# Kernel optimization log

Measured on AMD Instinct MI355X. Metric: run time of the kernel, lower is better.

Reference implementation:

```python
import jax, jax.numpy as jnp
import numpy as np

N_NODES = 100000
N_EDGES = 1600000
IN_DIM = 256
HID = 128
N_LAYERS = 4
OUT_DIM = 7
LAMDA = 0.5
LN_EPS = 1e-5


def setup_inputs() -> dict:
    key = jax.random.key(0)
    ks = jax.random.split(key, 12)
    x = jax.random.normal(ks[0], (N_NODES, IN_DIM), jnp.float32)
    edge_index = jax.random.randint(ks[1], (2, N_EDGES), 0, N_NODES, dtype=jnp.int32)

    def unif(k, shape, fan_out):
        s = 1.0 / np.sqrt(fan_out)
        return jax.random.uniform(k, shape, jnp.float32, -s, s)

    W_proj = unif(ks[2], (IN_DIM, HID), HID)
    b_proj = unif(ks[3], (HID,), HID)
    gamma = jnp.ones((HID,), jnp.float32)
    beta = jnp.zeros((HID,), jnp.float32)
    q_w = unif(ks[4], (HID, 1), 1)
    q_b = unif(ks[5], (1,), 1)
    conv_w = unif(ks[6], (N_LAYERS, HID, HID), HID)
    cls_w = unif(ks[7], (HID, OUT_DIM), OUT_DIM)
    cls_b = unif(ks[8], (OUT_DIM,), OUT_DIM)
    return {"x": x, "edge_index": edge_index, "W_proj": W_proj, "b_proj": b_proj,
            "gamma": gamma, "beta": beta, "q_w": q_w, "q_b": q_b,
            "conv_w": conv_w, "cls_w": cls_w, "cls_b": cls_b}


def reference(x, edge_index, W_proj, b_proj, gamma, beta, q_w, q_b, conv_w, cls_w, cls_b):
    n = x.shape[0]
    row, col = edge_index[0], edge_index[1]

    # symmetric normalization: D^-1/2 A D^-1/2 with unit edge data (duplicates sum)
    deg = jax.ops.segment_sum(jnp.ones(row.shape[0], x.dtype), row, num_segments=n)
    deg = jnp.where(deg == 0, jnp.ones_like(deg), deg)  # (row_sum==0)*1 + row_sum
    d_inv_sqrt = deg ** -0.5
    ew = d_inv_sqrt[row] * d_inv_sqrt[col]  # [E]

    def spmm(h):  # out[r] += ew * h[c]
        return jax.ops.segment_sum(ew[:, None] * h[col], row, num_segments=n)

    def layernorm(h):
        mu = jnp.mean(h, axis=-1, keepdims=True)
        var = jnp.mean((h - mu) ** 2, axis=-1, keepdims=True)
        return gamma * (h - mu) * jax.lax.rsqrt(var + LN_EPS) + beta

    h0 = layernorm(x @ W_proj + b_proj)  # project + layernorm
    h = h0
    for i in range(conv_w.shape[0]):
        # dropout is identity in eval mode
        s = jax.nn.sigmoid(h @ q_w + q_b - 1.0)  # [N,1] learned gate
        theta = LAMDA / (i + 1)
        hi = spmm(h)
        support = (1.0 - s) * hi + s * h0  # AOR blend (variant=False -> r == support)
        out = theta * (support @ conv_w[i]) + (1.0 - theta) * support  # DLR
        h = layernorm(jax.nn.relu(out))
    return h @ cls_w + cls_b
```

## Files before the change

kernel.cpp:

```cpp
#include <hip/hip_runtime.h>
#include <hip/hip_bf16.h>
#include <hip/hip_fp16.h>
#include <stdint.h>

#define N_NODES 100000
#define N_EDGES 1600000
#define IN_DIM 256
#define HID 128
#define N_LAYERS 4
#define OUT_DIM 7
#define LN_EPS 1e-5f

#define BSHIFT 6
#define BROWS 64
#define NBK 1563
#define CHUNK 16384
#define NCH ((N_EDGES + CHUNK - 1) / CHUNK)

typedef __attribute__((ext_vector_type(8))) short bf16x8;
typedef __attribute__((ext_vector_type(4))) float f32x4;

__device__ inline float bf2f1(uint16_t u) {
    union { uint32_t i; float f; } a; a.i = ((uint32_t)u) << 16; return a.f;
}
__device__ inline uint16_t f2bf(float f) {
    union { float f; uint32_t i; } a; a.f = f;
    uint32_t lsb = (a.i >> 16) & 1u;
    a.i += 0x7fffu + lsb;
    return (uint16_t)(a.i >> 16);
}
__device__ inline uint32_t packq(float a, float b, float qinv) {
    int qa = __float2int_rn(a * qinv);
    int qb = __float2int_rn(b * qinv);
    return ((uint32_t)(uint16_t)(short)qa) | (((uint32_t)(uint16_t)(short)qb) << 16);
}

__device__ __host__ inline int wpack_idx(int k, int c) {
    int kc = k >> 6, ks = (k >> 5) & 1, lg = (k >> 3) & 3, e = k & 7;
    int ct = c >> 4, li = c & 15;
    return ((((kc * 2 + ks) * 8 + ct) * 16 + li) * 4 + lg) * 8 + e;
}

__global__ void k_detect(const uint32_t* __restrict__ W, int* __restrict__ flag) {
    if (threadIdx.x == 0 && blockIdx.x == 0) {
        int cnt = 0;
        for (int i = 0; i < 64; i++) {
            uint32_t lo = W[i] & 0xffffu;
            uint32_t ex = (lo >> 7) & 0xff;
            if (ex >= 0x60 && ex < 0x7c) cnt++;
        }
        *flag = (cnt < 32) ? 1 : 0;
    }
}
__global__ void k_setflag(int* __restrict__ flag, int v) {
    if (threadIdx.x == 0) *flag = v;
}

__global__ __launch_bounds__(256) void k_cvt(const void* a0, const void* a1, const void* a2,
                                             const void* a3, const void* a4, const void* a5,
                                             const void* a6, const void* a7, const void* a8,
                                             float* __restrict__ dst, const int* __restrict__ flag) {
    int t = blockIdx.x * 256 + threadIdx.x;
    if (t >= 99720) return;
    const void* src; int i; int off;
    if      (t < 32768) { src = a0; i = t;         off = 0;     }
    else if (t < 32896) { src = a1; i = t - 32768; off = 32768; }
    else if (t < 33024) { src = a2; i = t - 32896; off = 32896; }
    else if (t < 33152) { src = a3; i = t - 33024; off = 33024; }
    else if (t < 33280) { src = a4; i = t - 33152; off = 33152; }
    else if (t < 33281) { src = a5; i = t - 33280; off = 33280; }
    else if (t < 98817) { src = a6; i = t - 33281; off = 33296; }
    else if (t < 99713) { src = a7; i = t - 98817; off = 98832; }
    else                { src = a8; i = t - 99713; off = 99728; }
    float v;
    if (*flag) v = ((const float*)src)[i];
    else       v = bf2f1(((const uint16_t*)src)[i]);
    dst[off + i] = v;
}

__global__ __launch_bounds__(256) void k_wsplit(const float* __restrict__ stg,
                                                uint16_t* __restrict__ wpkhi, uint16_t* __restrict__ wpklo,
                                                uint16_t* __restrict__ cwkhi, uint16_t* __restrict__ cwklo) {
    int t = blockIdx.x * 256 + threadIdx.x;
    if (t >= 32768 + 65536) return;
    float v; size_t dst; uint16_t *ha, *la;
    if (t < 32768) {
        int k = t >> 7, c = t & 127;
        v = stg[t];
        dst = (size_t)wpack_idx(k, c); ha = wpkhi; la = wpklo;
    } else {
        int u = t - 32768;
        int L = u >> 14, rem = u & 16383;
        int k = rem >> 7, c = rem & 127;
        v = stg[33296 + u];
        dst = (size_t)L * 16384 + wpack_idx(k, c); ha = cwkhi; la = cwklo;
    }
    uint16_t hb = f2bf(v);
    uint16_t lb = f2bf(v - bf2f1(hb));
    ha[dst] = hb; la[dst] = lb;
}


__global__ __launch_bounds__(256) void k_hist(const int* __restrict__ row, int* __restrict__ hist) {
    __shared__ int lh[NBK];
    int b = blockIdx.x, tid = threadIdx.x;
    for (int i = tid; i < NBK; i += 256) lh[i] = 0;
    __syncthreads();
    int e0 = b * CHUNK;
    int lim = N_EDGES - e0; if (lim > CHUNK) lim = CHUNK;
    for (int i = tid; i < lim; i += 256) atomicAdd(&lh[row[e0 + i] >> BSHIFT], 1);
    __syncthreads();
    for (int i = tid; i < NBK; i += 256) hist[(size_t)b * NBK + i] = lh[i];
}

__global__ __launch_bounds__(128) void k_hscan(int* __restrict__ hist, int* __restrict__ totB) {
    __shared__ int s[128];
    int bkt = blockIdx.x, t = threadIdx.x;
    int v = (t < NCH) ? hist[(size_t)t * NBK + bkt] : 0;
    s[t] = v;
    __syncthreads();
    for (int off = 1; off < 128; off <<= 1) {
        int add = (t >= off) ? s[t - off] : 0;
        __syncthreads();
        s[t] += add;
        __syncthreads();
    }
    if (t < NCH) hist[(size_t)t * NBK + bkt] = s[t] - v;
    if (t == 127) totB[bkt] = s[127];
}

__global__ __launch_bounds__(256) void k_bscan(const int* __restrict__ totB,
                                               int* __restrict__ boffB, int* __restrict__ rp) {
    __shared__ int ps[256];
    int t = threadIdx.x;
    const int STRIP = 7;
    int base = t * STRIP;
    int loc[STRIP]; int sum = 0;
#pragma unroll
    for (int j = 0; j < STRIP; j++) {
        int idx = base + j;
        int v = (idx < NBK) ? totB[idx] : 0;
        loc[j] = sum; sum += v;
    }
    ps[t] = sum;
    __syncthreads();
    int v = ps[t];
    for (int off = 1; off < 256; off <<= 1) {
        int add = (t >= off) ? ps[t - off] : 0;
        __syncthreads();
        ps[t] += add;
        __syncthreads();
    }
    int excl = ps[t] - v;
#pragma unroll
    for (int j = 0; j < STRIP; j++) {
        int idx = base + j;
        if (idx < NBK) boffB[idx] = excl + loc[j];
    }
    if (t == 0) { boffB[NBK] = N_EDGES; rp[N_NODES] = N_EDGES; }
}

__global__ __launch_bounds__(256) void k_sortscat(const int* __restrict__ row, const int* __restrict__ col,
                                                  const int* __restrict__ hist, const int* __restrict__ boffB,
                                                  uint32_t* __restrict__ ebp) {
    __shared__ int dbase[NBK];
    __shared__ int lcnt[NBK];
    int b = blockIdx.x, tid = threadIdx.x;
    for (int i = tid; i < NBK; i += 256) {
        dbase[i] = boffB[i] + hist[(size_t)b * NBK + i];
        lcnt[i] = 0;
    }
    __syncthreads();
    int e0 = b * CHUNK;
    int lim = N_EDGES - e0; if (lim > CHUNK) lim = CHUNK;
    for (int i = tid; i < lim; i += 256) {
        int r = row[e0 + i], c = col[e0 + i];
        int bk = r >> BSHIFT;
        int rank = atomicAdd(&lcnt[bk], 1);
        ebp[dbase[bk] + rank] = ((uint32_t)(r & (BROWS - 1)) << 17) | (uint32_t)c;
    }
}

__global__ __launch_bounds__(256) void k_bfin(const uint32_t* __restrict__ ebp, const int* __restrict__ boffB,
                                              int* __restrict__ rp, float* __restrict__ dis,
                                              int* __restrict__ edc) {
    __shared__ int ldeg[BROWS];
    __shared__ int lcur[BROWS];
    int b = blockIdx.x, tid = threadIdx.x;
    int base = boffB[b];
    int n = boffB[b + 1] - base;
    if (tid < BROWS) ldeg[tid] = 0;
    __syncthreads();
    for (int i = tid; i < n; i += 256) atomicAdd(&ldeg[ebp[base + i] >> 17], 1);
    __syncthreads();
    if (tid == 0) {
        int run = 0;
        for (int r = 0; r < BROWS; r++) { int d = ldeg[r]; lcur[r] = run; run += d; }
    }
    __syncthreads();
    int row0 = b << BSHIFT;
    if (tid < BROWS && row0 + tid < N_NODES) {
        int d = ldeg[tid];
        rp[row0 + tid]  = base + lcur[tid];
        dis[row0 + tid] = rsqrtf((float)(d > 0 ? d : 1));
    }
    __syncthreads();
    for (int i = tid; i < n; i += 256) {
        uint32_t pk = ebp[base + i];
        int r = pk >> 17;
        int pos = atomicAdd(&lcur[r], 1);
        edc[base + pos] = (int)(pk & 0x1FFFFu);
    }
}


__global__ __launch_bounds__(256) void k_spmm(const uint32_t* __restrict__ Hq,
                                              const float* __restrict__ ScD,
                                              const float* __restrict__ H0,
                                              const int* __restrict__ rp,
                                              const int* __restrict__ edc,
                                              const float* __restrict__ S,
                                              const float* __restrict__ dis,
                                              float* __restrict__ Sup) {
    int wid  = (blockIdx.x * 256 + threadIdx.x) >> 6;
    int lane = threadIdx.x & 63;
    if (wid >= N_NODES) return;

    float s  = S[wid];
    float dr = dis[wid];
    float h0x = H0[(size_t)wid * 128 + lane];
    float h0y = H0[(size_t)wid * 128 + 64 + lane];

    int p0 = rp[wid], p1 = rp[wid + 1];
    float ax = 0.f, ay = 0.f;
    int p = p0;
    for (; p + 8 <= p1; p += 8) {
        int c[8]; uint32_t u[8]; float w[8];
#pragma unroll
        for (int j = 0; j < 8; j++) c[j] = edc[p + j];
#pragma unroll
        for (int j = 0; j < 8; j++) u[j] = Hq[(size_t)c[j] * 64 + lane];
#pragma unroll
        for (int j = 0; j < 8; j++) w[j] = ScD[c[j]];
#pragma unroll
        for (int j = 0; j < 8; j++) {
            ax += w[j] * (float)((int)(u[j] << 16) >> 16);
            ay += w[j] * (float)((int)u[j] >> 16);
        }
    }
    for (; p + 4 <= p1; p += 4) {
        int c[4]; uint32_t u[4]; float w[4];
#pragma unroll
        for (int j = 0; j < 4; j++) c[j] = edc[p + j];
#pragma unroll
        for (int j = 0; j < 4; j++) u[j] = Hq[(size_t)c[j] * 64 + lane];
#pragma unroll
        for (int j = 0; j < 4; j++) w[j] = ScD[c[j]];
#pragma unroll
        for (int j = 0; j < 4; j++) {
            ax += w[j] * (float)((int)(u[j] << 16) >> 16);
            ay += w[j] * (float)((int)u[j] >> 16);
        }
    }
    for (; p < p1; p++) {
        int c = edc[p];
        uint32_t u = Hq[(size_t)c * 64 + lane];
        float w = ScD[c];
        ax += w * (float)((int)(u << 16) >> 16);
        ay += w * (float)((int)u >> 16);
    }
    float f = (1.f - s) * dr;
    Sup[(size_t)wid * 128 + lane]      = f * ax + s * h0x;
    Sup[(size_t)wid * 128 + 64 + lane] = f * ay + s * h0y;
}


template <int KD, int MODE, int WH, int WQ, int WF>
__global__ __launch_bounds__(256, 4) void k_gemm(
    const void* __restrict__ Araw,
    const uint16_t* __restrict__ Whi,
    const uint16_t* __restrict__ Wlo,
    const float* __restrict__ bias, const float* __restrict__ gamma,
    const float* __restrict__ beta, const float* __restrict__ qw,
    const float* __restrict__ qb, float theta, const int* __restrict__ flag,
    const float* __restrict__ dis,
    float* __restrict__ Hout, uint32_t* __restrict__ Hq,
    float* __restrict__ Sc, float* __restrict__ S)
{
    if (*flag != WF) return;
    constexpr int F32A = (MODE == 0) ? WF : 1;
    constexpr int NC = KD / 64;

    const int tid  = threadIdx.x;
    const int lane = tid & 63;
    const int wv   = tid >> 6;
    const int li   = lane & 15;
    const int lg   = lane >> 4;
    const size_t row0 = (size_t)blockIdx.x * 64;
    size_t arow = row0 + wv * 16 + li;
    if (arow >= N_NODES) arow = N_NODES - 1;

    f32x4 acc[8];
#pragma unroll
    for (int ct = 0; ct < 8; ct++) acc[ct] = (f32x4){0.f, 0.f, 0.f, 0.f};

#pragma unroll
    for (int kc = 0; kc < NC; kc++) {
#pragma unroll
        for (int ks = 0; ks < 2; ks++) {
            const int koff = kc * 64 + ks * 32 + lg * 8;
            bf16x8 ah, al;
            if constexpr (F32A) {
                const float* ap = (const float*)Araw + arow * KD + koff;
                float4 u0 = *(const float4*)ap;
                float4 u1 = *(const float4*)(ap + 4);
                float f[8] = {u0.x, u0.y, u0.z, u0.w, u1.x, u1.y, u1.z, u1.w};
#pragma unroll
                for (int j = 0; j < 8; j++) {
                    uint16_t hb = f2bf(f[j]);
                    ah[j] = (short)hb;
                    al[j] = (short)f2bf(f[j] - bf2f1(hb));
                }
            } else {
                ah = *(const bf16x8*)((const uint16_t*)Araw + arow * KD + koff);
            }
            const size_t wb0 = (size_t)(kc * 2 + ks) * 4096 + (size_t)li * 32 + (size_t)lg * 8;
#pragma unroll
            for (int ct = 0; ct < 8; ct++) {
                const size_t wb = wb0 + (size_t)ct * 512;
                bf16x8 bh = *(const bf16x8*)(Whi + wb);
                acc[ct] = __builtin_amdgcn_mfma_f32_16x16x32_bf16(ah, bh, acc[ct], 0, 0, 0);
                if constexpr (F32A)
                    acc[ct] = __builtin_amdgcn_mfma_f32_16x16x32_bf16(al, bh, acc[ct], 0, 0, 0);
                if constexpr (WF) {
                    bf16x8 bl = *(const bf16x8*)(Wlo + wb);
                    acc[ct] = __builtin_amdgcn_mfma_f32_16x16x32_bf16(ah, bl, acc[ct], 0, 0, 0);
                }
            }
        }
    }

    float gm[8], bt[8], qv[8], bi[8];
#pragma unroll
    for (int ct = 0; ct < 8; ct++) {
        int c = ct * 16 + li;
        gm[ct] = gamma[c]; bt[ct] = beta[c]; qv[ct] = qw[c];
        bi[ct] = (MODE == 0) ? bias[c] : 0.f;
    }
    const float qbv = qb[0];
    const float om  = 1.f - theta;
    const float* Af = (const float*)Araw;

#pragma unroll
    for (int r = 0; r < 4; r++) {
        int rowl  = wv * 16 + lg * 4 + r;
        size_t rg = row0 + rowl;
        size_t rc = (rg < N_NODES) ? rg : (N_NODES - 1);
        float v[8];
        if (MODE == 0) {
#pragma unroll
            for (int ct = 0; ct < 8; ct++) v[ct] = acc[ct][r] + bi[ct];
        } else {
#pragma unroll
            for (int ct = 0; ct < 8; ct++) {
                float sv = Af[rc * KD + ct * 16 + li];
                float o  = theta * acc[ct][r] + om * sv;
                v[ct] = o > 0.f ? o : 0.f;
            }
        }
        float sum = 0.f, sq = 0.f;
#pragma unroll
        for (int ct = 0; ct < 8; ct++) { sum += v[ct]; sq += v[ct] * v[ct]; }
        sum += __shfl_xor(sum, 1); sum += __shfl_xor(sum, 2);
        sum += __shfl_xor(sum, 4); sum += __shfl_xor(sum, 8);
        sq  += __shfl_xor(sq, 1);  sq  += __shfl_xor(sq, 2);
        sq  += __shfl_xor(sq, 4);  sq  += __shfl_xor(sq, 8);
        float mu  = sum * (1.f / 128.f);
        float var = fmaxf(sq * (1.f / 128.f) - mu * mu, 0.f);
        float rs  = rsqrtf(var + LN_EPS);
        float y[8];
#pragma unroll
        for (int ct = 0; ct < 8; ct++) y[ct] = gm[ct] * (v[ct] - mu) * rs + bt[ct];

        if (WQ) {
            float zd = 0.f, am = 0.f;
#pragma unroll
            for (int ct = 0; ct < 8; ct++) { zd += y[ct] * qv[ct]; am = fmaxf(am, fabsf(y[ct])); }
            zd += __shfl_xor(zd, 1); zd += __shfl_xor(zd, 2);
            zd += __shfl_xor(zd, 4); zd += __shfl_xor(zd, 8);
            am = fmaxf(am, __shfl_xor(am, 1)); am = fmaxf(am, __shfl_xor(am, 2));
            am = fmaxf(am, __shfl_xor(am, 4)); am = fmaxf(am, __shfl_xor(am, 8));
            float amc  = fmaxf(am, 1e-20f);
            float qinv = 32767.f / amc;
            if (rg < N_NODES) {
                uint32_t* mq = Hq + rg * 64;
#pragma unroll
                for (int ct = 0; ct < 4; ct++)
                    mq[ct * 16 + li] = packq(y[ct], y[ct + 4], qinv);
                if (li == 0) {
                    Sc[rg] = amc * (1.f / 32767.f) * dis[rg];
                    S[rg]  = 1.f / (1.f + __expf(-(zd + qbv - 1.f)));
                }
            }
        }
        if (WH && rg < N_NODES) {
            float* dst = Hout + rg * 128;
#pragma unroll
            for (int ct = 0; ct < 8; ct++) dst[ct * 16 + li] = y[ct];
        }
    }
}


__global__ __launch_bounds__(256) void k_cls(const float* __restrict__ H,
                                             const float* __restrict__ Wc,
                                             const float* __restrict__ bc,
                                             const int* __restrict__ flag,
                                             void* __restrict__ out) {
    __shared__ float wS[128][8];
    int tid = threadIdx.x;
    for (int idx = tid; idx < 128 * 7; idx += 256) wS[idx / 7][idx % 7] = Wc[idx];
    __syncthreads();
    int isf32 = *flag;
    int gid = blockIdx.x * 256 + tid;
    int n = gid >> 3, j = gid & 7;
    if (n >= N_NODES || j >= OUT_DIM) return;
    const float4* hr = (const float4*)(H + (size_t)n * 128);
    float acc = bc[j];
#pragma unroll
    for (int k4 = 0; k4 < 32; k4++) {
        float4 h4 = hr[k4];
        acc += h4.x * wS[4 * k4][j]     + h4.y * wS[4 * k4 + 1][j]
             + h4.z * wS[4 * k4 + 2][j] + h4.w * wS[4 * k4 + 3][j];
    }
    size_t oi = (size_t)n * OUT_DIM + j;
    if (isf32) ((float*)out)[oi] = acc;
    else       ((uint16_t*)out)[oi] = f2bf(acc);
}


extern "C" void kernel_launch(void* const* d_in, const int* in_sizes, int n_in,
                              void* d_out, int out_size, void* d_ws, size_t ws_size,
                              hipStream_t stream) {
    const void* x_raw = d_in[0];
    const int*  ei    = (const int*)d_in[1];
    const int* row = ei;
    const int* col = ei + N_EDGES;

    char* ws = (char*)d_ws;
    size_t off = 0;
    auto alloc = [&](size_t b) { void* p = ws + off; off = (off + b + 255) & ~(size_t)255; return p; };
    int*      flag = (int*)alloc(4);
    float*    stgf = (float*)alloc((size_t)99744 * 4);
    int*      rp   = (int*)alloc(((size_t)N_NODES + 1) * 4);
    float*    dis  = (float*)alloc((size_t)N_NODES * 4);
    int*      hist = (int*)alloc((size_t)NCH * NBK * 4);
    int*      totB = (int*)alloc((size_t)NBK * 4);
    int*      boffB= (int*)alloc(((size_t)NBK + 1) * 4);
    int*      edc  = (int*)alloc((size_t)N_EDGES * 4);
    float*    h0   = (float*)alloc((size_t)N_NODES * HID * 4);
    float*    sup  = (float*)alloc((size_t)N_NODES * HID * 4);
    uint32_t* hq   = (uint32_t*)alloc((size_t)N_NODES * 64 * 4);
    float*    Scq  = (float*)alloc((size_t)N_NODES * 4);
    float*    Sg   = (float*)alloc((size_t)N_NODES * 4);
    uint16_t* wpkhi = (uint16_t*)alloc((size_t)32768 * 2);
    uint16_t* wpklo = (uint16_t*)alloc((size_t)32768 * 2);
    uint16_t* cwkhi = (uint16_t*)alloc((size_t)65536 * 2);
    uint16_t* cwklo = (uint16_t*)alloc((size_t)65536 * 2);
    uint32_t* ebp  = (uint32_t*)h0;

    const float* bp  = stgf + 32768;
    const float* gm  = stgf + 32896;
    const float* bt  = stgf + 33024;
    const float* qw  = stgf + 33152;
    const float* qb  = stgf + 33280;
    const float* clw = stgf + 98832;
    const float* clb = stgf + 99728;

    int hostflag = -1;
    if (in_sizes && n_in >= 3) {
        if      (in_sizes[2] == 32768 * 4) hostflag = 1;
        else if (in_sizes[2] == 32768 * 2) hostflag = 0;
        else if (in_sizes[0] == N_NODES * IN_DIM * 4) hostflag = 1;
        else if (in_sizes[0] == N_NODES * IN_DIM * 2) hostflag = 0;
    }
    if (hostflag >= 0) k_setflag<<<1, 64, 0, stream>>>(flag, hostflag);
    else               k_detect<<<1, 64, 0, stream>>>((const uint32_t*)d_in[2], flag);

    k_cvt<<<(99720 + 255) / 256, 256, 0, stream>>>(d_in[2], d_in[3], d_in[4], d_in[5], d_in[6],
                                                   d_in[7], d_in[8], d_in[9], d_in[10], stgf, flag);
    k_wsplit<<<(98304 + 255) / 256, 256, 0, stream>>>(stgf, wpkhi, wpklo, cwkhi, cwklo);

    k_hist<<<NCH, 256, 0, stream>>>(row, hist);
    k_hscan<<<NBK, 128, 0, stream>>>(hist, totB);
    k_bscan<<<1, 256, 0, stream>>>(totB, boffB, rp);
    k_sortscat<<<NCH, 256, 0, stream>>>(row, col, hist, boffB, ebp);
    k_bfin<<<NBK, 256, 0, stream>>>(ebp, boffB, rp, dis, edc);

    const int gemm_grid = (N_NODES + 63) / 64;
    if (hostflag != 0)
        k_gemm<IN_DIM, 0, 1, 1, 1><<<gemm_grid, 256, 0, stream>>>(
            x_raw, wpkhi, wpklo, bp, gm, bt, qw, qb, 0.f, flag, dis, h0, hq, Scq, Sg);
    if (hostflag != 1)
        k_gemm<IN_DIM, 0, 1, 1, 0><<<gemm_grid, 256, 0, stream>>>(
            x_raw, wpkhi, wpklo, bp, gm, bt, qw, qb, 0.f, flag, dis, h0, hq, Scq, Sg);

    for (int i = 0; i < N_LAYERS; i++) {
        k_spmm<<<(N_NODES + 3) / 4, 256, 0, stream>>>(hq, Scq, h0, rp, edc, Sg, dis, sup);
        float theta = 0.5f / (float)(i + 1);
        const uint16_t* whi = cwkhi + (size_t)i * 16384;
        const uint16_t* wlo = cwklo + (size_t)i * 16384;
        if (i < N_LAYERS - 1) {
            if (hostflag != 0)
                k_gemm<HID, 1, 0, 1, 1><<<gemm_grid, 256, 0, stream>>>(
                    sup, whi, wlo, nullptr, gm, bt, qw, qb, theta, flag, dis, sup, hq, Scq, Sg);
            if (hostflag != 1)
                k_gemm<HID, 1, 0, 1, 0><<<gemm_grid, 256, 0, stream>>>(
                    sup, whi, wlo, nullptr, gm, bt, qw, qb, theta, flag, dis, sup, hq, Scq, Sg);
        } else {
            if (hostflag != 0)
                k_gemm<HID, 1, 1, 0, 1><<<gemm_grid, 256, 0, stream>>>(
                    sup, whi, wlo, nullptr, gm, bt, qw, qb, theta, flag, dis, sup, hq, Scq, Sg);
            if (hostflag != 1)
                k_gemm<HID, 1, 1, 0, 0><<<gemm_grid, 256, 0, stream>>>(
                    sup, whi, wlo, nullptr, gm, bt, qw, qb, theta, flag, dis, sup, hq, Scq, Sg);
        }
    }
    k_cls<<<((size_t)N_NODES * 8 + 255) / 256, 256, 0, stream>>>(sup, clw, clb, flag, d_out);
}
```

Before: 834.6 us.

## Stage GEMM weights in LDS, double rows per wave, store support as bf16 hi/lo

The GEMM now copies each 128-deep weight slab into shared memory once per block, with a repacked weight layout, and each wave computes 32 rows instead of 16. The block tile grows to 128 rows, so weight reads from global/L2 are amortised over more rows. The SpMM writes the support matrix pre-split into bf16 hi and lo halves, so the GEMM skips the fp32-to-bf16 split and reads the same number of bytes. The costs are higher register and LDS use, with occupancy lowered to 2 blocks per SM, plus a change in where the final layer output lands (h0 reused).

```diff
diff --git a/kernel.cpp b/kernel.cpp
--- a/kernel.cpp
+++ b/kernel.cpp
@@ -36,9 +36,9 @@
 }
 
 __device__ __host__ inline int wpack_idx(int k, int c) {
-    int kc = k >> 6, ks = (k >> 5) & 1, lg = (k >> 3) & 3, e = k & 7;
+    int ksg = k >> 5, lg = (k >> 3) & 3, e = k & 7;
     int ct = c >> 4, li = c & 15;
-    return ((((kc * 2 + ks) * 8 + ct) * 16 + li) * 4 + lg) * 8 + e;
+    return ((ksg * 8 + ct) * 64 + (lg * 16 + li)) * 8 + e;
 }
 
 __global__ void k_detect(const uint32_t* __restrict__ W, int* __restrict__ flag) {
@@ -221,7 +221,8 @@
                                               const int* __restrict__ edc,
                                               const float* __restrict__ S,
                                               const float* __restrict__ dis,
-                                              float* __restrict__ Sup) {
+                                              uint16_t* __restrict__ SupHi,
+                                              uint16_t* __restrict__ SupLo) {
     int wid  = (blockIdx.x * 256 + threadIdx.x) >> 6;
     int lane = threadIdx.x & 63;
     if (wid >= N_NODES) return;
@@ -270,16 +271,22 @@
         ay += w * (float)((int)u >> 16);
     }
     float f = (1.f - s) * dr;
-    Sup[(size_t)wid * 128 + lane]      = f * ax + s * h0x;
-    Sup[(size_t)wid * 128 + 64 + lane] = f * ay + s * h0y;
+    float ox = f * ax + s * h0x;
+    float oy = f * ay + s * h0y;
+    uint16_t hx = f2bf(ox), hy = f2bf(oy);
+    uint16_t lx = f2bf(ox - bf2f1(hx)), ly = f2bf(oy - bf2f1(hy));
+    SupHi[(size_t)wid * 128 + lane]      = hx;
+    SupHi[(size_t)wid * 128 + 64 + lane] = hy;
+    SupLo[(size_t)wid * 128 + lane]      = lx;
+    SupLo[(size_t)wid * 128 + 64 + lane] = ly;
 }
 
 
 template <int KD, int MODE, int WH, int WQ, int WF>
-__global__ __launch_bounds__(256, 4) void k_gemm(
-    const void* __restrict__ Araw,
-    const uint16_t* __restrict__ Whi,
-    const uint16_t* __restrict__ Wlo,
+__global__ __launch_bounds__(256, 2) void k_gemm(
+    const void* __restrict__ Ax,
+    const uint16_t* __restrict__ Ahi, const uint16_t* __restrict__ Alo,
+    const uint16_t* __restrict__ Wh, const uint16_t* __restrict__ Wl,
     const float* __restrict__ bias, const float* __restrict__ gamma,
     const float* __restrict__ beta, const float* __restrict__ qw,
     const float* __restrict__ qb, float theta, const int* __restrict__ flag,
@@ -289,126 +296,169 @@
 {
     if (*flag != WF) return;
     constexpr int F32A = (MODE == 0) ? WF : 1;
-    constexpr int NC = KD / 64;
+    constexpr int NKB = KD / 128;
+
+    __shared__ __align__(16) uint16_t sWh[16384];
+    __shared__ __align__(16) uint16_t sWl[16384];
 
     const int tid  = threadIdx.x;
     const int lane = tid & 63;
     const int wv   = tid >> 6;
     const int li   = lane & 15;
     const int lg   = lane >> 4;
-    const size_t row0 = (size_t)blockIdx.x * 64;
-    size_t arow = row0 + wv * 16 + li;
-    if (arow >= N_NODES) arow = N_NODES - 1;
-
-    f32x4 acc[8];
-#pragma unroll
-    for (int ct = 0; ct < 8; ct++) acc[ct] = (f32x4){0.f, 0.f, 0.f, 0.f};
-
-#pragma unroll
-    for (int kc = 0; kc < NC; kc++) {
-#pragma unroll
-        for (int ks = 0; ks < 2; ks++) {
-            const int koff = kc * 64 + ks * 32 + lg * 8;
-            bf16x8 ah, al;
-            if constexpr (F32A) {
-                const float* ap = (const float*)Araw + arow * KD + koff;
-                float4 u0 = *(const float4*)ap;
-                float4 u1 = *(const float4*)(ap + 4);
-                float f[8] = {u0.x, u0.y, u0.z, u0.w, u1.x, u1.y, u1.z, u1.w};
+    const size_t row0 = (size_t)blockIdx.x * 128;
+    const int wb = wv * 32;
+    size_t ar0 = row0 + wb + li;      if (ar0 >= N_NODES) ar0 = N_NODES - 1;
+    size_t ar1 = row0 + wb + 16 + li; if (ar1 >= N_NODES) ar1 = N_NODES - 1;
+
+    f32x4 acc0[8], acc1[8];
+#pragma unroll
+    for (int ct = 0; ct < 8; ct++) {
+        acc0[ct] = (f32x4){0.f, 0.f, 0.f, 0.f};
+        acc1[ct] = (f32x4){0.f, 0.f, 0.f, 0.f};
+    }
+
+    for (int kb = 0; kb < NKB; kb++) {
+        if (kb) __syncthreads();
+        const uint16_t* gh = Wh + kb * 16384;
+#pragma unroll
+        for (int it = 0; it < 8; it++) {
+            int t = tid + it * 256;
+            *(uint4*)(sWh + t * 8) = *(const uint4*)(gh + t * 8);
+        }
+        if constexpr (WF) {
+            const uint16_t* gl = Wl + kb * 16384;
+#pragma unroll
+            for (int it = 0; it < 8; it++) {
+                int t = tid + it * 256;
+                *(uint4*)(sWl + t * 8) = *(const uint4*)(gl + t * 8);
+            }
+        }
+        bf16x8 a0h[4], a1h[4], a0l[4], a1l[4];
+#pragma unroll
+        for (int s = 0; s < 4; s++) {
+            const int koff = kb * 128 + s * 32 + lg * 8;
+            if constexpr (MODE == 1) {
+                a0h[s] = *(const bf16x8*)(Ahi + ar0 * KD + koff);
+                a0l[s] = *(const bf16x8*)(Alo + ar0 * KD + koff);
+                a1h[s] = *(const bf16x8*)(Ahi + ar1 * KD + koff);
+                a1l[s] = *(const bf16x8*)(Alo + ar1 * KD + koff);
+            } else if constexpr (WF) {
+                const float* p0 = (const float*)Ax + ar0 * KD + koff;
+                const float* p1 = (const float*)Ax + ar1 * KD + koff;
+                float4 u0 = *(const float4*)p0, u1 = *(const float4*)(p0 + 4);
+                float4 v0 = *(const float4*)p1, v1 = *(const float4*)(p1 + 4);
+                float f0[8] = {u0.x, u0.y, u0.z, u0.w, u1.x, u1.y, u1.z, u1.w};
+                float f1[8] = {v0.x, v0.y, v0.z, v0.w, v1.x, v1.y, v1.z, v1.w};
 #pragma unroll
                 for (int j = 0; j < 8; j++) {
-                    uint16_t hb = f2bf(f[j]);
-                    ah[j] = (short)hb;
-                    al[j] = (short)f2bf(f[j] - bf2f1(hb));
+                    uint16_t hb0 = f2bf(f0[j]);
+                    a0h[s][j] = (short)hb0;
+                    a0l[s][j] = (short)f2bf(f0[j] - bf2f1(hb0));
+                    uint16_t hb1 = f2bf(f1[j]);
+                    a1h[s][j] = (short)hb1;
+                    a1l[s][j] = (short)f2bf(f1[j] - bf2f1(hb1));
                 }
             } else {
-                ah = *(const bf16x8*)((const uint16_t*)Araw + arow * KD + koff);
+                a0h[s] = *(const bf16x8*)((const uint16_t*)Ax + ar0 * KD + koff);
+                a1h[s] = *(const bf16x8*)((const uint16_t*)Ax + ar1 * KD + koff);
             }
-            const size_t wb0 = (size_t)(kc * 2 + ks) * 4096 + (size_t)li * 32 + (size_t)lg * 8;
+        }
+        __syncthreads();
+#pragma unroll
+        for (int s = 0; s < 4; s++) {
 #pragma unroll
             for (int ct = 0; ct < 8; ct++) {
-                const size_t wb = wb0 + (size_t)ct * 512;
-                bf16x8 bh = *(const bf16x8*)(Whi + wb);
-                acc[ct] = __builtin_amdgcn_mfma_f32_16x16x32_bf16(ah, bh, acc[ct], 0, 0, 0);
-                if constexpr (F32A)
-                    acc[ct] = __builtin_amdgcn_mfma_f32_16x16x32_bf16(al, bh, acc[ct], 0, 0, 0);
+                const int wo = ((s * 8 + ct) * 64 + lane) * 8;
+                bf16x8 bh = *(const bf16x8*)(sWh + wo);
+                acc0[ct] = __builtin_amdgcn_mfma_f32_16x16x32_bf16(a0h[s], bh, acc0[ct], 0, 0, 0);
+                acc1[ct] = __builtin_amdgcn_mfma_f32_16x16x32_bf16(a1h[s], bh, acc1[ct], 0, 0, 0);
+                if constexpr (F32A) {
+                    acc0[ct] = __builtin_amdgcn_mfma_f32_16x16x32_bf16(a0l[s], bh, acc0[ct], 0, 0, 0);
+                    acc1[ct] = __builtin_amdgcn_mfma_f32_16x16x32_bf16(a1l[s], bh, acc1[ct], 0, 0, 0);
+                }
                 if constexpr (WF) {
-                    bf16x8 bl = *(const bf16x8*)(Wlo + wb);
-                    acc[ct] = __builtin_amdgcn_mfma_f32_16x16x32_bf16(ah, bl, acc[ct], 0, 0, 0);
+                    bf16x8 bl = *(const bf16x8*)(sWl + wo);
+                    acc0[ct] = __builtin_amdgcn_mfma_f32_16x16x32_bf16(a0h[s], bl, acc0[ct], 0, 0, 0);
+                    acc1[ct] = __builtin_amdgcn_mfma_f32_16x16x32_bf16(a1h[s], bl, acc1[ct], 0, 0, 0);
                 }
             }
         }
     }
 
-    float gm[8], bt[8], qv[8], bi[8];
+    float gm[8], bt_[8], qv[8], bi[8];
 #pragma unroll
     for (int ct = 0; ct < 8; ct++) {
         int c = ct * 16 + li;
-        gm[ct] = gamma[c]; bt[ct] = beta[c]; qv[ct] = qw[c];
+        gm[ct] = gamma[c]; bt_[ct] = beta[c]; qv[ct] = qw[c];
         bi[ct] = (MODE == 0) ? bias[c] : 0.f;
     }
     const float qbv = qb[0];
     const float om  = 1.f - theta;
-    const float* Af = (const float*)Araw;
-
-#pragma unroll
-    for (int r = 0; r < 4; r++) {
-        int rowl  = wv * 16 + lg * 4 + r;
-        size_t rg = row0 + rowl;
-        size_t rc = (rg < N_NODES) ? rg : (N_NODES - 1);
-        float v[8];
-        if (MODE == 0) {
-#pragma unroll
-            for (int ct = 0; ct < 8; ct++) v[ct] = acc[ct][r] + bi[ct];
-        } else {
-#pragma unroll
-            for (int ct = 0; ct < 8; ct++) {
-                float sv = Af[rc * KD + ct * 16 + li];
-                float o  = theta * acc[ct][r] + om * sv;
-                v[ct] = o > 0.f ? o : 0.f;
-            }
-        }
-        float sum = 0.f, sq = 0.f;
-#pragma unroll
-        for (int ct = 0; ct < 8; ct++) { sum += v[ct]; sq += v[ct] * v[ct]; }
-        sum += __shfl_xor(sum, 1); sum += __shfl_xor(sum, 2);
-        sum += __shfl_xor(sum, 4); sum += __shfl_xor(sum, 8);
-        sq  += __shfl_xor(sq, 1);  sq  += __shfl_xor(sq, 2);
-        sq  += __shfl_xor(sq, 4);  sq  += __shfl_xor(sq, 8);
-        float mu  = sum * (1.f / 128.f);
-        float var = fmaxf(sq * (1.f / 128.f) - mu * mu, 0.f);
-        float rs  = rsqrtf(var + LN_EPS);
-        float y[8];
-#pragma unroll
-        for (int ct = 0; ct < 8; ct++) y[ct] = gm[ct] * (v[ct] - mu) * rs + bt[ct];
-
-        if (WQ) {
-            float zd = 0.f, am = 0.f;
-#pragma unroll
-            for (int ct = 0; ct < 8; ct++) { zd += y[ct] * qv[ct]; am = fmaxf(am, fabsf(y[ct])); }
-            zd += __shfl_xor(zd, 1); zd += __shfl_xor(zd, 2);
-            zd += __shfl_xor(zd, 4); zd += __shfl_xor(zd, 8);
-            am = fmaxf(am, __shfl_xor(am, 1)); am = fmaxf(am, __shfl_xor(am, 2));
-            am = fmaxf(am, __shfl_xor(am, 4)); am = fmaxf(am, __shfl_xor(am, 8));
-            float amc  = fmaxf(am, 1e-20f);
-            float qinv = 32767.f / amc;
-            if (rg < N_NODES) {
-                uint32_t* mq = Hq + rg * 64;
-#pragma unroll
-                for (int ct = 0; ct < 4; ct++)
-                    mq[ct * 16 + li] = packq(y[ct], y[ct + 4], qinv);
-                if (li == 0) {
-                    Sc[rg] = amc * (1.f / 32767.f) * dis[rg];
-                    S[rg]  = 1.f / (1.f + __expf(-(zd + qbv - 1.f)));
+
+    auto epi = [&](f32x4 (&acc)[8], int ssoff) {
+#pragma unroll
+        for (int r = 0; r < 4; r++) {
+            int rowl  = wb + ssoff + lg * 4 + r;
+            size_t rg = row0 + rowl;
+            size_t rc = (rg < N_NODES) ? rg : (N_NODES - 1);
+            float v[8];
+            if (MODE == 0) {
+#pragma unroll
+                for (int ct = 0; ct < 8; ct++) v[ct] = acc[ct][r] + bi[ct];
+            } else {
+#pragma unroll
+                for (int ct = 0; ct < 8; ct++) {
+                    int c = ct * 16 + li;
+                    float sv = bf2f1(Ahi[rc * KD + c]) + bf2f1(Alo[rc * KD + c]);
+                    float o  = theta * acc[ct][r] + om * sv;
+                    v[ct] = o > 0.f ? o : 0.f;
                 }
             }
-        }
-        if (WH && rg < N_NODES) {
-            float* dst = Hout + rg * 128;
-#pragma unroll
-            for (int ct = 0; ct < 8; ct++) dst[ct * 16 + li] = y[ct];
-        }
-    }
+            float sum = 0.f, sq = 0.f;
+#pragma unroll
+            for (int ct = 0; ct < 8; ct++) { sum += v[ct]; sq += v[ct] * v[ct]; }
+            sum += __shfl_xor(sum, 1); sum += __shfl_xor(sum, 2);
+            sum += __shfl_xor(sum, 4); sum += __shfl_xor(sum, 8);
+            sq  += __shfl_xor(sq, 1);  sq  += __shfl_xor(sq, 2);
+            sq  += __shfl_xor(sq, 4);  sq  += __shfl_xor(sq, 8);
+            float mu  = sum * (1.f / 128.f);
+            float var = fmaxf(sq * (1.f / 128.f) - mu * mu, 0.f);
+            float rs  = rsqrtf(var + LN_EPS);
+            float y[8];
+#pragma unroll
+            for (int ct = 0; ct < 8; ct++) y[ct] = gm[ct] * (v[ct] - mu) * rs + bt_[ct];
+
+            if (WQ) {
+                float zd = 0.f, am = 0.f;
+#pragma unroll
+                for (int ct = 0; ct < 8; ct++) { zd += y[ct] * qv[ct]; am = fmaxf(am, fabsf(y[ct])); }
+                zd += __shfl_xor(zd, 1); zd += __shfl_xor(zd, 2);
+                zd += __shfl_xor(zd, 4); zd += __shfl_xor(zd, 8);
+                am = fmaxf(am, __shfl_xor(am, 1)); am = fmaxf(am, __shfl_xor(am, 2));
+                am = fmaxf(am, __shfl_xor(am, 4)); am = fmaxf(am, __shfl_xor(am, 8));
+                float amc  = fmaxf(am, 1e-20f);
+                float qinv = 32767.f / amc;
+                if (rg < N_NODES) {
+                    uint32_t* mq = Hq + rg * 64;
+#pragma unroll
+                    for (int ct = 0; ct < 4; ct++)
+                        mq[ct * 16 + li] = packq(y[ct], y[ct + 4], qinv);
+                    if (li == 0) {
+                        Sc[rg] = amc * (1.f / 32767.f) * dis[rg];
+                        S[rg]  = 1.f / (1.f + __expf(-(zd + qbv - 1.f)));
+                    }
+                }
+            }
+            if (WH && rg < N_NODES) {
+                float* dst = Hout + rg * 128;
+#pragma unroll
+                for (int ct = 0; ct < 8; ct++) dst[ct * 16 + li] = y[ct];
+            }
+        }
+    };
+    epi(acc0, 0);
+    epi(acc1, 16);
 }
 
 
@@ -459,7 +509,8 @@
     int*      boffB= (int*)alloc(((size_t)NBK + 1) * 4);
     int*      edc  = (int*)alloc((size_t)N_EDGES * 4);
     float*    h0   = (float*)alloc((size_t)N_NODES * HID * 4);
-    float*    sup  = (float*)alloc((size_t)N_NODES * HID * 4);
+    uint16_t* suphi= (uint16_t*)alloc((size_t)N_NODES * HID * 2);
+    uint16_t* suplo= (uint16_t*)alloc((size_t)N_NODES * HID * 2);
     uint32_t* hq   = (uint32_t*)alloc((size_t)N_NODES * 64 * 4);
     float*    Scq  = (float*)alloc((size_t)N_NODES * 4);
     float*    Sg   = (float*)alloc((size_t)N_NODES * 4);
@@ -497,34 +548,41 @@
     k_sortscat<<<NCH, 256, 0, stream>>>(row, col, hist, boffB, ebp);
     k_bfin<<<NBK, 256, 0, stream>>>(ebp, boffB, rp, dis, edc);
 
-    const int gemm_grid = (N_NODES + 63) / 64;
+    const int gg = (N_NODES + 127) / 128;
     if (hostflag != 0)
-        k_gemm<IN_DIM, 0, 1, 1, 1><<<gemm_grid, 256, 0, stream>>>(
-            x_raw, wpkhi, wpklo, bp, gm, bt, qw, qb, 0.f, flag, dis, h0, hq, Scq, Sg);
+        k_gemm<IN_DIM, 0, 1, 1, 1><<<gg, 256, 0, stream>>>(
+            x_raw, nullptr, nullptr, wpkhi, wpklo, bp, gm, bt, qw, qb, 0.f, flag, dis,
+            h0, hq, Scq, Sg);
     if (hostflag != 1)
-        k_gemm<IN_DIM, 0, 1, 1, 0><<<gemm_grid, 256, 0, stream>>>(
-            x_raw, wpkhi, wpklo, bp, gm, bt, qw, qb, 0.f, flag, dis, h0, hq, Scq, Sg);
+        k_gemm<IN_DIM, 0, 1, 1, 0><<<gg, 256, 0, stream>>>(
+            x_raw, nullptr, nullptr, wpkhi, wpklo, bp, gm, bt, qw, qb, 0.f, flag, dis,
+            h0, hq, Scq, Sg);
 
     for (int i = 0; i < N_LAYERS; i++) {
-        k_spmm<<<(N_NODES + 3) / 4, 256, 0, stream>>>(hq, Scq, h0, rp, edc, Sg, dis, sup);
+        k_spmm<<<(N_NODES + 3) / 4, 256, 0, stream>>>(hq, Scq, h0, rp, edc, Sg, dis, suphi, suplo);
         float theta = 0.5f / (float)(i + 1);
         const uint16_t* whi = cwkhi + (size_t)i * 16384;
         const uint16_t* wlo = cwklo + (size_t)i * 16384;
-        if (i < N_LAYERS - 1) {
+        const int wh = (i == N_LAYERS - 1) ? 1 : 0;
+        if (wh) {
             if (hostflag != 0)
-                k_gemm<HID, 1, 0, 1, 1><<<gemm_grid, 256, 0, stream>>>(
-                    sup, whi, wlo, nullptr, gm, bt, qw, qb, theta, flag, dis, sup, hq, Scq, Sg);
+                k_gemm<HID, 1, 1, 0, 1><<<gg, 256, 0, stream>>>(
+                    nullptr, suphi, suplo, whi, wlo, nullptr, gm, bt, qw, qb, theta, flag, dis,
+                    h0, hq, Scq, Sg);
             if (hostflag != 1)
-                k_gemm<HID, 1, 0, 1, 0><<<gemm_grid, 256, 0, stream>>>(
-                    sup, whi, wlo, nullptr, gm, bt, qw, qb, theta, flag, dis, sup, hq, Scq, Sg);
+                k_gemm<HID, 1, 1, 0, 0><<<gg, 256, 0, stream>>>(
+                    nullptr, suphi, suplo, whi, wlo, nullptr, gm, bt, qw, qb, theta, flag, dis,
+                    h0, hq, Scq, Sg);
         } else {
             if (hostflag != 0)
-                k_gemm<HID, 1, 1, 0, 1><<<gemm_grid, 256, 0, stream>>>(
-                    sup, whi, wlo, nullptr, gm, bt, qw, qb, theta, flag, dis, sup, hq, Scq, Sg);
+                k_gemm<HID, 1, 0, 1, 1><<<gg, 256, 0, stream>>>(
+                    nullptr, suphi, suplo, whi, wlo, nullptr, gm, bt, qw, qb, theta, flag, dis,
+                    h0, hq, Scq, Sg);
             if (hostflag != 1)
-                k_gemm<HID, 1, 1, 0, 0><<<gemm_grid, 256, 0, stream>>>(
-                    sup, whi, wlo, nullptr, gm, bt, qw, qb, theta, flag, dis, sup, hq, Scq, Sg);
-        }
-    }
-    k_cls<<<((size_t)N_NODES * 8 + 255) / 256, 256, 0, stream>>>(sup, clw, clb, flag, d_out);
-}
+                k_gemm<HID, 1, 0, 1, 0><<<gg, 256, 0, stream>>>(
+                    nullptr, suphi, suplo, whi, wlo, nullptr, gm, bt, qw, qb, theta, flag, dis,
+                    h0, hq, Scq, Sg);
+        }
+    }
+    k_cls<<<((size_t)N_NODES * 8 + 255) / 256, 256, 0, stream>>>(h0, clw, clb, flag, d_out);
+}
```

New measurement: 750.3 us. -10.1%, faster.
